# Optimization experiments

Hardware: AMD Instinct MI355X
Metric: run time of the kernel (lower is better)

The kernel has to match this reference:

```python
import jax, jax.numpy as jnp
import numpy as np

B, H, W, C = 32, 64, 64, 256
NH, WS, SHIFT = 8, 8, 4
HD = C // NH
N = WS * WS           # tokens per window
NW = (H // WS) * (W // WS)
HID = 4 * C
EPS_LN = 1e-5
LOGIT_MAX = float(np.log(1.0 / 0.01))


def _rel_coords_table():
    ch = np.arange(-(WS - 1), WS, dtype=np.float32)
    t = np.stack(np.meshgrid(ch, ch, indexing='ij'), axis=-1)  # (2WS-1, 2WS-1, 2)
    t = t / (WS - 1) * 8.0
    t = np.sign(t) * np.log2(np.abs(t) + 1.0) / np.log2(8.0)
    return t.reshape(-1, 2)  # ((2WS-1)^2, 2)


def _rel_pos_index():
    coords = np.stack(np.meshgrid(np.arange(WS), np.arange(WS), indexing='ij'))
    cf = coords.reshape(2, -1)
    rel = (cf[:, :, None] - cf[:, None, :]).transpose(1, 2, 0).copy()
    rel[:, :, 0] += WS - 1
    rel[:, :, 1] += WS - 1
    rel[:, :, 0] *= 2 * WS - 1
    return rel.sum(-1)  # (N, N) int


def _attn_mask():
    img = np.zeros((H, W), np.float32)
    cnt = 0
    for hs in (slice(0, -WS), slice(-WS, -SHIFT), slice(-SHIFT, None)):
        for ws in (slice(0, -WS), slice(-WS, -SHIFT), slice(-SHIFT, None)):
            img[hs, ws] = cnt
            cnt += 1
    mw = img.reshape(H // WS, WS, W // WS, WS).transpose(0, 2, 1, 3).reshape(-1, N)
    diff = mw[:, None, :] - mw[:, :, None]
    return np.where(diff != 0, -100.0, 0.0).astype(np.float32)  # (NW, N, N)


_RCT = jnp.asarray(_rel_coords_table())
_RPI = jnp.asarray(_rel_pos_index())
_MASK = jnp.asarray(_attn_mask())


def _ln(x, g, b):
    mu = jnp.mean(x, axis=-1, keepdims=True)
    var = jnp.mean(jnp.square(x - mu), axis=-1, keepdims=True)
    return (x - mu) * jax.lax.rsqrt(var + EPS_LN) * g + b


def _l2n(x):
    return x / jnp.sqrt(jnp.maximum(jnp.sum(x * x, axis=-1, keepdims=True), 1e-12))


def setup_inputs() -> dict:
    key = jax.random.key(0)
    ks = jax.random.split(key, 16)
    s = 0.02
    return {
        'x': jax.random.normal(ks[0], (B, H * W, C), jnp.float32),
        'qkv_w': jax.random.normal(ks[1], (C, 3 * C), jnp.float32) * s,
        'q_bias': jnp.zeros((C,), jnp.float32),
        'v_bias': jnp.zeros((C,), jnp.float32),
        'logit_scale': jnp.full((NH, 1, 1), np.log(10.0), jnp.float32),
        'cpb_w1': jax.random.normal(ks[2], (2, 512), jnp.float32) * s,
        'cpb_b1': jnp.zeros((512,), jnp.float32),
        'cpb_w2': jax.random.normal(ks[3], (512, NH), jnp.float32) * s,
        'proj_w': jax.random.normal(ks[4], (C, C), jnp.float32) * s,
        'proj_b': jnp.zeros((C,), jnp.float32),
        'norm1_g': jnp.ones((C,), jnp.float32),
        'norm1_b': jnp.zeros((C,), jnp.float32),
        'fc1_w': jax.random.normal(ks[5], (C, HID), jnp.float32) * s,
        'fc1_b': jnp.zeros((HID,), jnp.float32),
        'fc2_w': jax.random.normal(ks[6], (HID, C), jnp.float32) * s,
        'fc2_b': jnp.zeros((C,), jnp.float32),
        'norm2_g': jnp.ones((C,), jnp.float32),
        'norm2_b': jnp.zeros((C,), jnp.float32),
    }


def reference(x, qkv_w, q_bias, v_bias, logit_scale, cpb_w1, cpb_b1, cpb_w2,
              proj_w, proj_b, norm1_g, norm1_b, fc1_w, fc1_b, fc2_w, fc2_b,
              norm2_g, norm2_b):
    shortcut = x
    xs = x.reshape(B, H, W, C)
    # cyclic shift
    xs = jnp.roll(xs, shift=(-SHIFT, -SHIFT), axis=(1, 2))
    # window partition -> (B*NW, N, C)
    xw = xs.reshape(B, H // WS, WS, W // WS, WS, C).transpose(0, 1, 3, 2, 4, 5)
    xw = xw.reshape(B * NW, N, C)

    # qkv projection (kernel without bias, then split q/v biases, k bias zero)
    qkv_bias = jnp.concatenate([q_bias, jnp.zeros_like(q_bias), v_bias], axis=0)
    qkv = xw @ qkv_w + qkv_bias
    qkv = qkv.reshape(B * NW, N, 3, NH, HD).transpose(2, 0, 3, 1, 4)
    q, k, v = qkv[0], qkv[1], qkv[2]  # (B*NW, NH, N, HD)

    # cosine attention
    attn = jnp.einsum('bhnd,bhmd->bhnm', _l2n(q), _l2n(k))
    scale = jnp.exp(jnp.minimum(logit_scale, LOGIT_MAX))  # (NH,1,1)
    attn = attn * scale

    # CPB-MLP relative position bias
    table = jax.nn.relu(_RCT @ cpb_w1 + cpb_b1) @ cpb_w2          # ((2WS-1)^2, NH)
    bias = table[_RPI]                                            # (N, N, NH)
    bias = 16.0 * jax.nn.sigmoid(bias.transpose(2, 0, 1))         # (NH, N, N)
    attn = attn + bias[None]

    # shifted-window mask
    attn = attn.reshape(B, NW, NH, N, N) + _MASK[None, :, None]
    attn = jax.nn.softmax(attn.reshape(B * NW, NH, N, N), axis=-1)

    out = jnp.einsum('bhnm,bhmd->bhnd', attn, v)
    out = out.transpose(0, 2, 1, 3).reshape(B * NW, N, C)
    out = out @ proj_w + proj_b

    # window reverse + reverse shift
    out = out.reshape(B, H // WS, W // WS, WS, WS, C).transpose(0, 1, 3, 2, 4, 5)
    out = out.reshape(B, H, W, C)
    out = jnp.roll(out, shift=(SHIFT, SHIFT), axis=(1, 2)).reshape(B, H * W, C)

    # SwinV2 post-norm residuals
    x = shortcut + _ln(out, norm1_g, norm1_b)
    h = jax.nn.gelu(x @ fc1_w + fc1_b, approximate=False) @ fc2_w + fc2_b
    x = x + _ln(h, norm2_g, norm2_b)
    return x
```

## Files before the change

kernel.cpp:

```cpp
#include <hip/hip_runtime.h>


#define TOKS 131072
#define LOGIT_MAX 4.60517018598809136804f

typedef __attribute__((ext_vector_type(8))) short short8;
typedef __attribute__((ext_vector_type(4))) float f32x4;

__device__ __forceinline__ float b2f(unsigned short s) {
    union { unsigned int u; float f; } x; x.u = ((unsigned int)s) << 16; return x.f;
}
__device__ __forceinline__ unsigned short f2b(float f) {
    union { float f; unsigned int u; } x; x.f = f;
    unsigned int r = x.u + 0x7fffu + ((x.u >> 16) & 1u);
    return (unsigned short)(r >> 16);
}

#define MFMA16(a, b, c) __builtin_amdgcn_mfma_f32_16x16x32_bf16((a), (b), (c), 0, 0, 0)

#define GLOAD_LDS16(g, l)                                                      \
    __builtin_amdgcn_global_load_lds(                                          \
        (const __attribute__((address_space(1))) void*)(g),                    \
        (__attribute__((address_space(3))) void*)(l), 16, 0, 0)


__global__ __launch_bounds__(256) void cvt_kernel(const float* __restrict__ in,
                                                  unsigned short* __restrict__ out, int n) {
    int i = (blockIdx.x * 256 + threadIdx.x) * 4;
    if (i >= n) return;
    float4 v = *(const float4*)(in + i);
    ushort4 o;
    o.x = f2b(v.x); o.y = f2b(v.y); o.z = f2b(v.z); o.w = f2b(v.w);
    *(ushort4*)(out + i) = o;
}

__global__ __launch_bounds__(256) void wt_kernel(const float* __restrict__ src,
                                                 unsigned short* __restrict__ dst,
                                                 int K, int N) {
    int idx = blockIdx.x * 256 + threadIdx.x;
    if (idx >= K * N) return;
    int n = idx / K, k = idx - n * K;
    dst[idx] = f2b(src[(size_t)k * N + n]);
}

__device__ __forceinline__ float cpb_coord(int d) {
    float t = (float)d * (8.0f / 7.0f);
    float a = log2f(fabsf(t) + 1.0f) * (1.0f / 3.0f);
    return t < 0.0f ? -a : a;
}

__global__ __launch_bounds__(256) void cpb_kernel(
    const float* __restrict__ w1, const float* __restrict__ b1, const float* __restrict__ w2,
    const float* __restrict__ qb, const float* __restrict__ vb,
    float* __restrict__ biasT, float* __restrict__ qkv_bias)
{
    __shared__ float tbl[225];
    int h = blockIdx.x, t = threadIdx.x;
    if (t < 225) {
        float r0 = cpb_coord(t / 15 - 7), r1 = cpb_coord(t % 15 - 7);
        float acc = 0.f;
        for (int j = 0; j < 512; ++j) {
            float hid = fmaxf(r0 * w1[j] + r1 * w1[512 + j] + b1[j], 0.f);
            acc += hid * w2[j * 8 + h];
        }
        tbl[t] = acc;
    }
    __syncthreads();
    for (int o = t; o < 4096; o += 256) {
        int i = o >> 6, j = o & 63;
        int idx = ((i >> 3) - (j >> 3) + 7) * 15 + ((i & 7) - (j & 7) + 7);
        biasT[h * 4096 + o] = 16.0f / (1.0f + __expf(-tbl[idx]));
    }
    if (h == 0)
        for (int n = t; n < 768; n += 256)
            qkv_bias[n] = n < 256 ? qb[n] : (n < 512 ? 0.f : vb[n - 512]);
}

template<int EPI>
__global__ __launch_bounds__(256) void gemm_bt(
    const unsigned short* __restrict__ A, const unsigned short* __restrict__ Bt,
    const float* __restrict__ bias, unsigned short* __restrict__ out,
    int M, int N, int K)
{
    __shared__ __align__(16) unsigned short sA[128 * 32];
    __shared__ __align__(16) unsigned short sB[128 * 32];
    const int tid = threadIdx.x;
    const int lane = tid & 63;
    const int wave = tid >> 6;
    const int wm = (wave >> 1) * 64, wn = (wave & 1) * 64;
    const int m0 = blockIdx.y * 128, n0 = blockIdx.x * 128;
    const int l15 = lane & 15, lq = lane >> 4;
    const int r0 = tid >> 2, c0 = (tid & 3) << 3;

    f32x4 acc[4][4] = {};
    const size_t arow0 = (size_t)(m0 + r0) * K + c0;
    const size_t arow1 = (size_t)(m0 + r0 + 64) * K + c0;
    const size_t brow0 = (size_t)(n0 + r0) * K + c0;
    const size_t brow1 = (size_t)(n0 + r0 + 64) * K + c0;
    unsigned short* dA0 = sA + wave * 512;
    unsigned short* dA1 = sA + 2048 + wave * 512;
    unsigned short* dB0 = sB + wave * 512;
    unsigned short* dB1 = sB + 2048 + wave * 512;

    for (int k0 = 0; k0 < K; k0 += 32) {
        GLOAD_LDS16(A + arow0 + k0, dA0);
        GLOAD_LDS16(A + arow1 + k0, dA1);
        GLOAD_LDS16(Bt + brow0 + k0, dB0);
        GLOAD_LDS16(Bt + brow1 + k0, dB1);
        __syncthreads();
        short8 af[4], bw[4];
        #pragma unroll
        for (int t = 0; t < 4; ++t) {
            af[t] = *(const short8*)&sA[(wm + t * 16 + l15) * 32 + lq * 8];
            bw[t] = *(const short8*)&sB[(wn + t * 16 + l15) * 32 + lq * 8];
        }
        #pragma unroll
        for (int tm = 0; tm < 4; ++tm)
            #pragma unroll
            for (int tn = 0; tn < 4; ++tn)
                acc[tm][tn] = MFMA16(af[tm], bw[tn], acc[tm][tn]);
        __syncthreads();
    }

    #pragma unroll
    for (int tm = 0; tm < 4; ++tm)
        #pragma unroll
        for (int tn = 0; tn < 4; ++tn)
            #pragma unroll
            for (int r = 0; r < 4; ++r) {
                int gm = m0 + wm + tm * 16 + lq * 4 + r;
                int gn = n0 + wn + tn * 16 + l15;
                float v = acc[tm][tn][r] + bias[gn];
                if constexpr (EPI == 2)
                    v = 0.5f * v * (1.0f + erff(v * 0.70710678118654752f));
                if constexpr (EPI == 1) {
                    int s = gn >> 8, hd = gn & 255;
                    out[((size_t)(s * 8 + (hd >> 5)) * TOKS + gm) * 32 + (hd & 31)] = f2b(v);
                } else {
                    out[(size_t)gm * N + gn] = f2b(v);
                }
            }
}


__device__ __forceinline__ int regid(int wy, int wx, int t) {
    int y = wy * 8 + (t >> 3), x = wx * 8 + (t & 7);
    int ry = (y < 56) ? 0 : (y < 60 ? 1 : 2);
    int rx = (x < 56) ? 0 : (x < 60 ? 1 : 2);
    return ry * 3 + rx;
}

__device__ __forceinline__ void load_norm(const unsigned short* __restrict__ p,
                                          unsigned short* __restrict__ dst, int lane) {
    union U { uint4 u; unsigned short s[8]; };
    U ld[4];
    #pragma unroll
    for (int c = 0; c < 4; ++c) ld[c].u = *(const uint4*)(p + c * 8);
    float f[32]; float ss = 0.f;
    #pragma unroll
    for (int c = 0; c < 4; ++c)
        #pragma unroll
        for (int j = 0; j < 8; ++j) { float v = b2f(ld[c].s[j]); f[c * 8 + j] = v; ss += v * v; }
    float nrm = rsqrtf(fmaxf(ss, 1e-12f));
    #pragma unroll
    for (int c = 0; c < 4; ++c) {
        U st;
        #pragma unroll
        for (int j = 0; j < 8; ++j) st.s[j] = f2b(f[c * 8 + j] * nrm);
        *(uint4*)(dst + lane * 32 + c * 8) = st.u;
    }
}

__global__ __launch_bounds__(64) void attn_kernel(
    const unsigned short* __restrict__ qkv, const float* __restrict__ biasT,
    const float* __restrict__ ls, unsigned short* __restrict__ outb)
{
    __shared__ __align__(16) unsigned short sQ[64 * 32];
    __shared__ __align__(16) unsigned short sK[64 * 32];
    __shared__ __align__(16) unsigned short sV[64 * 32];
    __shared__ __align__(16) unsigned short sP[64 * 64];

    const int lane = threadIdx.x;
    const int h = blockIdx.x & 7;
    const int win = blockIdx.x >> 3;
    const int b = win >> 6;
    const int wy = (win >> 3) & 7, wx = win & 7;
    const int l15 = lane & 15, lq = lane >> 4;

    {
        int ty = lane >> 3, tx = lane & 7;
        int hh = (wy * 8 + ty + 4) & 63, ww = (wx * 8 + tx + 4) & 63;
        size_t tok = (size_t)b * 4096 + hh * 64 + ww;
        const size_t plane = (size_t)TOKS * 32;
        const unsigned short* qp = qkv + (size_t)h * plane + tok * 32;
        const unsigned short* kp = qkv + (size_t)(8 + h) * plane + tok * 32;
        const unsigned short* vp = qkv + (size_t)(16 + h) * plane + tok * 32;
        load_norm(qp, sQ, lane);
        load_norm(kp, sK, lane);
        #pragma unroll
        for (int c = 0; c < 4; ++c)
            *(uint4*)&sV[lane * 32 + c * 8] = *(const uint4*)(vp + c * 8);
    }
    __syncthreads();

    short8 aQ[4], bK[4];
    #pragma unroll
    for (int t = 0; t < 4; ++t) {
        aQ[t] = *(const short8*)&sQ[(t * 16 + l15) * 32 + lq * 8];
        bK[t] = *(const short8*)&sK[(t * 16 + l15) * 32 + lq * 8];
    }
    f32x4 acc[4][4] = {};
    #pragma unroll
    for (int tm = 0; tm < 4; ++tm)
        #pragma unroll
        for (int tn = 0; tn < 4; ++tn)
            acc[tm][tn] = MFMA16(aQ[tm], bK[tn], acc[tm][tn]);

    float scale = __expf(fminf(ls[h], LOGIT_MAX));

    #pragma unroll
    for (int tm = 0; tm < 4; ++tm)
        #pragma unroll
        for (int r = 0; r < 4; ++r) {
            int i = tm * 16 + lq * 4 + r;
            int ri = regid(wy, wx, i);
            float v[4];
            #pragma unroll
            for (int tn = 0; tn < 4; ++tn) {
                int j = tn * 16 + l15;
                float sc = acc[tm][tn][r] * scale + biasT[h * 4096 + i * 64 + j];
                if (ri != regid(wy, wx, j)) sc -= 100.f;
                v[tn] = sc;
            }
            float m = fmaxf(fmaxf(v[0], v[1]), fmaxf(v[2], v[3]));
            #pragma unroll
            for (int o = 1; o < 16; o <<= 1) m = fmaxf(m, __shfl_xor(m, o));
            float sum = 0.f;
            #pragma unroll
            for (int tn = 0; tn < 4; ++tn) { v[tn] = __expf(v[tn] - m); sum += v[tn]; }
            #pragma unroll
            for (int o = 1; o < 16; o <<= 1) sum += __shfl_xor(sum, o);
            float inv = 1.0f / sum;
            #pragma unroll
            for (int tn = 0; tn < 4; ++tn)
                sP[i * 64 + tn * 16 + l15] = f2b(v[tn] * inv);
        }
    __syncthreads();

    f32x4 accO[4][2] = {};
    #pragma unroll
    for (int ks = 0; ks < 2; ++ks) {
        short8 bV[2];
        #pragma unroll
        for (int tn = 0; tn < 2; ++tn)
            #pragma unroll
            for (int jj = 0; jj < 8; ++jj)
                bV[tn][jj] = (short)sV[(ks * 32 + lq * 8 + jj) * 32 + tn * 16 + l15];
        #pragma unroll
        for (int tm = 0; tm < 4; ++tm) {
            short8 aP = *(const short8*)&sP[(tm * 16 + l15) * 64 + ks * 32 + lq * 8];
            accO[tm][0] = MFMA16(aP, bV[0], accO[tm][0]);
            accO[tm][1] = MFMA16(aP, bV[1], accO[tm][1]);
        }
    }

    #pragma unroll
    for (int tm = 0; tm < 4; ++tm)
        #pragma unroll
        for (int r = 0; r < 4; ++r) {
            int i = tm * 16 + lq * 4 + r;
            int hh = (wy * 8 + (i >> 3) + 4) & 63, ww = (wx * 8 + (i & 7) + 4) & 63;
            size_t rowo = ((size_t)b * 4096 + hh * 64 + ww) * 256 + h * 32;
            outb[rowo + l15] = f2b(accO[tm][0][r]);
            outb[rowo + 16 + l15] = f2b(accO[tm][1][r]);
        }
}

template<int MODE>
__global__ __launch_bounds__(256) void ln_kernel(
    const unsigned short* __restrict__ src,
    const float* __restrict__ residf, const unsigned short* __restrict__ residb,
    const float* __restrict__ g, const float* __restrict__ be,
    unsigned short* __restrict__ outb, float* __restrict__ outf)
{
    const int row = blockIdx.x * 4 + (threadIdx.x >> 6);
    const int lane = threadIdx.x & 63;
    const size_t base = (size_t)row * 256 + lane * 4;
    ushort4 sv = *(const ushort4*)(src + base);
    float v[4] = { b2f(sv.x), b2f(sv.y), b2f(sv.z), b2f(sv.w) };
    float s = v[0] + v[1] + v[2] + v[3];
    float q = v[0] * v[0] + v[1] * v[1] + v[2] * v[2] + v[3] * v[3];
    #pragma unroll
    for (int o = 1; o < 64; o <<= 1) { s += __shfl_xor(s, o); q += __shfl_xor(q, o); }
    float mu = s * (1.0f / 256.0f);
    float var = q * (1.0f / 256.0f) - mu * mu;
    float rs = rsqrtf(var + 1e-5f);
    float4 gg = *(const float4*)(g + lane * 4);
    float4 bb = *(const float4*)(be + lane * 4);
    float gv[4] = { gg.x, gg.y, gg.z, gg.w }, bv[4] = { bb.x, bb.y, bb.z, bb.w };
    if constexpr (MODE == 1) {
        float4 rr = *(const float4*)(residf + base);
        float rv[4] = { rr.x, rr.y, rr.z, rr.w };
        ushort4 o;
        o.x = f2b(rv[0] + (v[0] - mu) * rs * gv[0] + bv[0]);
        o.y = f2b(rv[1] + (v[1] - mu) * rs * gv[1] + bv[1]);
        o.z = f2b(rv[2] + (v[2] - mu) * rs * gv[2] + bv[2]);
        o.w = f2b(rv[3] + (v[3] - mu) * rs * gv[3] + bv[3]);
        *(ushort4*)(outb + base) = o;
    } else {
        ushort4 rb = *(const ushort4*)(residb + base);
        float4 o;
        o.x = b2f(rb.x) + (v[0] - mu) * rs * gv[0] + bv[0];
        o.y = b2f(rb.y) + (v[1] - mu) * rs * gv[1] + bv[1];
        o.z = b2f(rb.z) + (v[2] - mu) * rs * gv[2] + bv[2];
        o.w = b2f(rb.w) + (v[3] - mu) * rs * gv[3] + bv[3];
        *(float4*)(outf + base) = o;
    }
}


extern "C" void kernel_launch(void* const* d_in, const int* in_sizes, int n_in,
                              void* d_out, int out_size, void* d_ws, size_t ws_size,
                              hipStream_t stream) {
    (void)in_sizes; (void)n_in; (void)out_size; (void)ws_size;
    const float* x      = (const float*)d_in[0];
    const float* qkv_w  = (const float*)d_in[1];
    const float* q_bias = (const float*)d_in[2];
    const float* v_bias = (const float*)d_in[3];
    const float* lscale = (const float*)d_in[4];
    const float* cpb_w1 = (const float*)d_in[5];
    const float* cpb_b1 = (const float*)d_in[6];
    const float* cpb_w2 = (const float*)d_in[7];
    const float* proj_w = (const float*)d_in[8];
    const float* proj_b = (const float*)d_in[9];
    const float* n1g    = (const float*)d_in[10];
    const float* n1b    = (const float*)d_in[11];
    const float* fc1_w  = (const float*)d_in[12];
    const float* fc1_b  = (const float*)d_in[13];
    const float* fc2_w  = (const float*)d_in[14];
    const float* fc2_b  = (const float*)d_in[15];
    const float* n2g    = (const float*)d_in[16];
    const float* n2b    = (const float*)d_in[17];

    char* ws = (char*)d_ws;
    unsigned short* R1 = (unsigned short*)(ws);
    unsigned short* R2 = (unsigned short*)(ws + 268435456);
    unsigned short* R3 = (unsigned short*)(ws + 335544320);
    unsigned short* qkv_wT = (unsigned short*)(ws + 402653184);
    unsigned short* proj_wT = (unsigned short*)(ws + 403046400);
    unsigned short* fc1_wT  = (unsigned short*)(ws + 403177472);
    unsigned short* fc2_wT  = (unsigned short*)(ws + 403701760);
    float* qkv_bias = (float*)(ws + 404226048);
    float* biasT    = (float*)(ws + 404229120);

    cvt_kernel<<<TOKS * 256 / 1024, 256, 0, stream>>>(x, R2, TOKS * 256);
    wt_kernel<<<(256 * 768 + 255) / 256, 256, 0, stream>>>(qkv_w, qkv_wT, 256, 768);
    wt_kernel<<<(256 * 256 + 255) / 256, 256, 0, stream>>>(proj_w, proj_wT, 256, 256);
    wt_kernel<<<(256 * 1024 + 255) / 256, 256, 0, stream>>>(fc1_w, fc1_wT, 256, 1024);
    wt_kernel<<<(1024 * 256 + 255) / 256, 256, 0, stream>>>(fc2_w, fc2_wT, 1024, 256);
    cpb_kernel<<<8, 256, 0, stream>>>(cpb_w1, cpb_b1, cpb_w2, q_bias, v_bias, biasT, qkv_bias);

    gemm_bt<1><<<dim3(6, TOKS / 128), 256, 0, stream>>>(R2, qkv_wT, qkv_bias, R1, TOKS, 768, 256);
    attn_kernel<<<16384, 64, 0, stream>>>(R1, biasT, lscale, R2);
    gemm_bt<0><<<dim3(2, TOKS / 128), 256, 0, stream>>>(R2, proj_wT, proj_b, R1, TOKS, 256, 256);
    ln_kernel<1><<<TOKS / 4, 256, 0, stream>>>(R1, x, nullptr, n1g, n1b, R3, nullptr);
    gemm_bt<2><<<dim3(8, TOKS / 128), 256, 0, stream>>>(R3, fc1_wT, fc1_b, R1, TOKS, 1024, 256);
    gemm_bt<0><<<dim3(2, TOKS / 128), 256, 0, stream>>>(R1, fc2_wT, fc2_b, R2, TOKS, 256, 1024);
    ln_kernel<2><<<TOKS / 4, 256, 0, stream>>>(R2, nullptr, R3, n2g, n2b, nullptr, (float*)d_out);
}
```

Before: 944.8 us.

## Fuse proj/fc2 GEMMs with LayerNorm residual, swizzle blocks, use tanh-style GELU

Adds a gemm_ln kernel that computes a full 256-wide output row tile per block and applies bias, LayerNorm and the residual add in the epilogue. It replaces the proj/fc2 GEMMs plus the separate LN kernels and removes the bf16 round trip of the intermediate. The generic GEMM also gets an XCD-style block swizzle and a hoisted bias load. The exact erf GELU is replaced by a sigmoid-form tanh approximation, which changes numerics slightly. The fused kernel's 64x256 tile stages more B data per block and loses the 2-D grid parallelism of the old GEMM.

```diff
diff --git a/kernel.cpp b/kernel.cpp
--- a/kernel.cpp
+++ b/kernel.cpp
@@ -88,7 +88,12 @@
     const int lane = tid & 63;
     const int wave = tid >> 6;
     const int wm = (wave >> 1) * 64, wn = (wave & 1) * 64;
-    const int m0 = blockIdx.y * 128, n0 = blockIdx.x * 128;
+    const int nwg = (int)(gridDim.x * gridDim.y);
+    int flat = (int)(blockIdx.y * gridDim.x + blockIdx.x);
+    flat = (flat & 7) * (nwg >> 3) + (flat >> 3);
+    const int bx = flat % (int)gridDim.x;
+    const int by = flat / (int)gridDim.x;
+    const int m0 = by * 128, n0 = bx * 128;
     const int l15 = lane & 15, lq = lane >> 4;
     const int r0 = tid >> 2, c0 = (tid & 3) << 3;
 
@@ -122,6 +127,10 @@
         __syncthreads();
     }
 
+    float bv[4];
+    #pragma unroll
+    for (int tn = 0; tn < 4; ++tn) bv[tn] = bias[n0 + wn + tn * 16 + l15];
+
     #pragma unroll
     for (int tm = 0; tm < 4; ++tm)
         #pragma unroll
@@ -130,9 +139,11 @@
             for (int r = 0; r < 4; ++r) {
                 int gm = m0 + wm + tm * 16 + lq * 4 + r;
                 int gn = n0 + wn + tn * 16 + l15;
-                float v = acc[tm][tn][r] + bias[gn];
-                if constexpr (EPI == 2)
-                    v = 0.5f * v * (1.0f + erff(v * 0.70710678118654752f));
+                float v = acc[tm][tn][r] + bv[tn];
+                if constexpr (EPI == 2) {
+                    float u = v * (1.5957691216057308f + 0.0713548162972754f * v * v);
+                    v = v / (1.0f + __expf(-u));
+                }
                 if constexpr (EPI == 1) {
                     int s = gn >> 8, hd = gn & 255;
                     out[((size_t)(s * 8 + (hd >> 5)) * TOKS + gm) * 32 + (hd & 31)] = f2b(v);
@@ -140,6 +151,103 @@
                     out[(size_t)gm * N + gn] = f2b(v);
                 }
             }
+}
+
+template<int MODE>
+__global__ __launch_bounds__(256) void gemm_ln(
+    const unsigned short* __restrict__ A, const unsigned short* __restrict__ Bt,
+    const float* __restrict__ bias,
+    const float* __restrict__ residf, const unsigned short* __restrict__ residb,
+    const float* __restrict__ lng, const float* __restrict__ lnb,
+    unsigned short* __restrict__ outb, float* __restrict__ outf, int K)
+{
+    __shared__ __align__(16) unsigned short sA[64 * 32];
+    __shared__ __align__(16) unsigned short sB[256 * 32];
+    const int tid = threadIdx.x;
+    const int lane = tid & 63;
+    const int wave = tid >> 6;
+    const int wn = wave * 64;
+    const int m0 = blockIdx.x * 64;
+    const int l15 = lane & 15, lq = lane >> 4;
+    const int r0 = tid >> 2, c0 = (tid & 3) << 3;
+
+    f32x4 acc[4][4] = {};
+    const size_t arow = (size_t)(m0 + r0) * K + c0;
+    const size_t brow = (size_t)r0 * K + c0;
+    unsigned short* dA  = sA + wave * 512;
+    unsigned short* dB0 = sB + wave * 512;
+    unsigned short* dB1 = sB + 2048 + wave * 512;
+    unsigned short* dB2 = sB + 4096 + wave * 512;
+    unsigned short* dB3 = sB + 6144 + wave * 512;
+
+    for (int k0 = 0; k0 < K; k0 += 32) {
+        GLOAD_LDS16(A + arow + k0, dA);
+        GLOAD_LDS16(Bt + brow + k0, dB0);
+        GLOAD_LDS16(Bt + brow + (size_t)64 * K + k0, dB1);
+        GLOAD_LDS16(Bt + brow + (size_t)128 * K + k0, dB2);
+        GLOAD_LDS16(Bt + brow + (size_t)192 * K + k0, dB3);
+        __syncthreads();
+        short8 af[4], bw[4];
+        #pragma unroll
+        for (int t = 0; t < 4; ++t) {
+            af[t] = *(const short8*)&sA[(t * 16 + l15) * 32 + lq * 8];
+            bw[t] = *(const short8*)&sB[(wn + t * 16 + l15) * 32 + lq * 8];
+        }
+        #pragma unroll
+        for (int tm = 0; tm < 4; ++tm)
+            #pragma unroll
+            for (int tn = 0; tn < 4; ++tn)
+                acc[tm][tn] = MFMA16(af[tm], bw[tn], acc[tm][tn]);
+        __syncthreads();
+    }
+
+    float bv[4], gv[4], ev[4];
+    #pragma unroll
+    for (int tn = 0; tn < 4; ++tn) {
+        int gn = wn + tn * 16 + l15;
+        bv[tn] = bias[gn]; gv[tn] = lng[gn]; ev[tn] = lnb[gn];
+    }
+
+    float* sums = (float*)sA;
+    float* sqs  = (float*)sA + 256;
+    #pragma unroll
+    for (int tm = 0; tm < 4; ++tm)
+        #pragma unroll
+        for (int r = 0; r < 4; ++r) {
+            int rl = tm * 16 + lq * 4 + r;
+            float s = 0.f, q = 0.f;
+            #pragma unroll
+            for (int tn = 0; tn < 4; ++tn) {
+                float v = acc[tm][tn][r] + bv[tn];
+                s += v; q += v * v;
+            }
+            #pragma unroll
+            for (int o = 1; o < 16; o <<= 1) { s += __shfl_xor(s, o); q += __shfl_xor(q, o); }
+            if (l15 == 0) { sums[rl * 4 + wave] = s; sqs[rl * 4 + wave] = q; }
+        }
+    __syncthreads();
+
+    #pragma unroll
+    for (int tm = 0; tm < 4; ++tm)
+        #pragma unroll
+        for (int r = 0; r < 4; ++r) {
+            int rl = tm * 16 + lq * 4 + r;
+            float s = sums[rl * 4] + sums[rl * 4 + 1] + sums[rl * 4 + 2] + sums[rl * 4 + 3];
+            float q = sqs[rl * 4] + sqs[rl * 4 + 1] + sqs[rl * 4 + 2] + sqs[rl * 4 + 3];
+            float mu = s * (1.0f / 256.0f);
+            float rs = rsqrtf(q * (1.0f / 256.0f) - mu * mu + 1e-5f);
+            size_t rowo = (size_t)(m0 + rl) * 256;
+            #pragma unroll
+            for (int tn = 0; tn < 4; ++tn) {
+                int gn = wn + tn * 16 + l15;
+                float v = acc[tm][tn][r] + bv[tn];
+                float nv = (v - mu) * rs * gv[tn] + ev[tn];
+                if constexpr (MODE == 1)
+                    outb[rowo + gn] = f2b(residf[rowo + gn] + nv);
+                else
+                    outf[rowo + gn] = b2f(residb[rowo + gn]) + nv;
+            }
+        }
 }
 
 
@@ -274,48 +382,6 @@
             outb[rowo + l15] = f2b(accO[tm][0][r]);
             outb[rowo + 16 + l15] = f2b(accO[tm][1][r]);
         }
-}
-
-template<int MODE>
-__global__ __launch_bounds__(256) void ln_kernel(
-    const unsigned short* __restrict__ src,
-    const float* __restrict__ residf, const unsigned short* __restrict__ residb,
-    const float* __restrict__ g, const float* __restrict__ be,
-    unsigned short* __restrict__ outb, float* __restrict__ outf)
-{
-    const int row = blockIdx.x * 4 + (threadIdx.x >> 6);
-    const int lane = threadIdx.x & 63;
-    const size_t base = (size_t)row * 256 + lane * 4;
-    ushort4 sv = *(const ushort4*)(src + base);
-    float v[4] = { b2f(sv.x), b2f(sv.y), b2f(sv.z), b2f(sv.w) };
-    float s = v[0] + v[1] + v[2] + v[3];
-    float q = v[0] * v[0] + v[1] * v[1] + v[2] * v[2] + v[3] * v[3];
-    #pragma unroll
-    for (int o = 1; o < 64; o <<= 1) { s += __shfl_xor(s, o); q += __shfl_xor(q, o); }
-    float mu = s * (1.0f / 256.0f);
-    float var = q * (1.0f / 256.0f) - mu * mu;
-    float rs = rsqrtf(var + 1e-5f);
-    float4 gg = *(const float4*)(g + lane * 4);
-    float4 bb = *(const float4*)(be + lane * 4);
-    float gv[4] = { gg.x, gg.y, gg.z, gg.w }, bv[4] = { bb.x, bb.y, bb.z, bb.w };
-    if constexpr (MODE == 1) {
-        float4 rr = *(const float4*)(residf + base);
-        float rv[4] = { rr.x, rr.y, rr.z, rr.w };
-        ushort4 o;
-        o.x = f2b(rv[0] + (v[0] - mu) * rs * gv[0] + bv[0]);
-        o.y = f2b(rv[1] + (v[1] - mu) * rs * gv[1] + bv[1]);
-        o.z = f2b(rv[2] + (v[2] - mu) * rs * gv[2] + bv[2]);
-        o.w = f2b(rv[3] + (v[3] - mu) * rs * gv[3] + bv[3]);
-        *(ushort4*)(outb + base) = o;
-    } else {
-        ushort4 rb = *(const ushort4*)(residb + base);
-        float4 o;
-        o.x = b2f(rb.x) + (v[0] - mu) * rs * gv[0] + bv[0];
-        o.y = b2f(rb.y) + (v[1] - mu) * rs * gv[1] + bv[1];
-        o.z = b2f(rb.z) + (v[2] - mu) * rs * gv[2] + bv[2];
-        o.w = b2f(rb.w) + (v[3] - mu) * rs * gv[3] + bv[3];
-        *(float4*)(outf + base) = o;
-    }
 }
 
 
@@ -362,9 +428,9 @@
 
     gemm_bt<1><<<dim3(6, TOKS / 128), 256, 0, stream>>>(R2, qkv_wT, qkv_bias, R1, TOKS, 768, 256);
     attn_kernel<<<16384, 64, 0, stream>>>(R1, biasT, lscale, R2);
-    gemm_bt<0><<<dim3(2, TOKS / 128), 256, 0, stream>>>(R2, proj_wT, proj_b, R1, TOKS, 256, 256);
-    ln_kernel<1><<<TOKS / 4, 256, 0, stream>>>(R1, x, nullptr, n1g, n1b, R3, nullptr);
+    gemm_ln<1><<<TOKS / 64, 256, 0, stream>>>(R2, proj_wT, proj_b, x, nullptr,
+                                              n1g, n1b, R3, nullptr, 256);
     gemm_bt<2><<<dim3(8, TOKS / 128), 256, 0, stream>>>(R3, fc1_wT, fc1_b, R1, TOKS, 1024, 256);
-    gemm_bt<0><<<dim3(2, TOKS / 128), 256, 0, stream>>>(R1, fc2_wT, fc2_b, R2, TOKS, 256, 1024);
-    ln_kernel<2><<<TOKS / 4, 256, 0, stream>>>(R2, nullptr, R3, n2g, n2b, nullptr, (float*)d_out);
-}
+    gemm_ln<2><<<TOKS / 64, 256, 0, stream>>>(R1, fc2_wT, fc2_b, nullptr, R3,
+                                              n2g, n2b, nullptr, (float*)d_out, 1024);
+}
```

Result: slower. 985.4 us (+4.3%).
